# Kernel optimization log

Hardware: AMD Instinct MI355X
Metric: run time of the kernel (lower is better)

Reference implementation:

```python
import jax, jax.numpy as jnp
import numpy as np

B, S, D = 4, 1024, 768
H = 12
DK = D // H            # 64
NUM_EMB = 10
MAX_DIST = 100000.0 * 2 ** 0.5
POS_SCALE = 100000.0   # tile positions live in [0, 100000]


def setup_inputs() -> dict:
    key = jax.random.key(0)
    ks = jax.random.split(key, 12)
    query = jax.random.normal(ks[0], (B, S, D), dtype=jnp.float32)
    key_t = jax.random.normal(ks[1], (B, S, D), dtype=jnp.float32)
    value = jax.random.normal(ks[2], (B, S, D), dtype=jnp.float32)
    tile_positions = jax.random.uniform(ks[3], (B, S, 2), dtype=jnp.float32) * POS_SCALE
    # Linear weights, torch layout [out, in]; xavier_uniform init, zero bias
    lim = float(np.sqrt(6.0 / (D + D)))
    Wq = jax.random.uniform(ks[4], (D, D), minval=-lim, maxval=lim, dtype=jnp.float32)
    Wk = jax.random.uniform(ks[5], (D, D), minval=-lim, maxval=lim, dtype=jnp.float32)
    Wv = jax.random.uniform(ks[6], (D, D), minval=-lim, maxval=lim, dtype=jnp.float32)
    bq = jnp.zeros((D,), jnp.float32)
    bk = jnp.zeros((D,), jnp.float32)
    bv = jnp.zeros((D,), jnp.float32)
    emb_k = jax.random.normal(ks[7], (NUM_EMB, DK), dtype=jnp.float32)  # nn.Embedding default N(0,1)
    return {"query": query, "key": key_t, "value": value,
            "tile_positions": tile_positions,
            "Wq": Wq, "bq": bq, "Wk": Wk, "bk": bk, "Wv": Wv, "bv": bv,
            "emb_k": emb_k}


def reference(query, key, value, tile_positions, Wq, bq, Wk, bk, Wv, bv, emb_k):
    b, s, _ = query.shape
    # projections -> [B, H, S, DK]
    q = (query @ Wq.T + bq).reshape(b, s, H, DK).transpose(0, 2, 1, 3)
    k = (key   @ Wk.T + bk).reshape(b, s, H, DK).transpose(0, 2, 1, 3)
    v = (value @ Wv.T + bv).reshape(b, s, H, DK).transpose(0, 2, 1, 3)
    # pairwise distances, normalized, discretized to embedding indices
    pos = jax.lax.stop_gradient(tile_positions)
    diff = pos[:, :, None, :] - pos[:, None, :, :]          # [B,S,S,2]
    dist = jnp.sqrt(jnp.sum(diff * diff, axis=-1)) / MAX_DIST  # [B,S,S]
    idx = jnp.clip(jnp.round(dist * (NUM_EMB - 1)), 0, NUM_EMB - 1).astype(jnp.int32)
    rk = emb_k[idx]                                          # [B,S,S,DK]
    # logits: QK^T plus distance-aware key bias
    attn_logits = jnp.einsum('bhqd,bhkd->bhqk', q, k)
    attn_logits = attn_logits + jnp.einsum('bhqd,bqkd->bhqk', q, rk)
    attn_logits = attn_logits / (DK ** 0.5)
    attention = jax.nn.softmax(attn_logits, axis=-1)
    out = jnp.einsum('bhqk,bhkd->bhqd', attention, v)       # [B,H,S,DK]
    out = out.transpose(0, 2, 1, 3).reshape(b, s, -1)       # [B,S,D]
    return out
```

## Files before the change

kernel.cpp:

```cpp
#include <hip/hip_runtime.h>
#include <hip/hip_bf16.h>

#define Bsz 4
#define Ssz 1024
#define Dsz 768
#define Hn 12
#define DKsz 64
#define NUMEMB 10

#define IDX_OFF 64
#define K_OFF   4194368
#define V_OFF   10485824
#define WBF_OFF 16777280
#define XBF_OFF 20316224
#define WS_TIER_B 20316224ULL
#define WS_TIER_A 39190592ULL

#define NXz 3145728
#define NWz 589824

typedef __attribute__((ext_vector_type(8))) short short8;
typedef __attribute__((ext_vector_type(8))) float float8;
typedef __attribute__((ext_vector_type(4))) float f32x4;
typedef __attribute__((ext_vector_type(4))) unsigned int u32x4;
typedef __attribute__((ext_vector_type(4))) short s16x4;

__device__ __forceinline__ float bfbits2f(short u) {
    union { unsigned int i; float f; } v;
    v.i = ((unsigned int)(unsigned short)u) << 16;
    return v.f;
}
__device__ __forceinline__ unsigned short f2bf_bits(float f) {
    __hip_bfloat16 h = __float2bfloat16(f);
    return *reinterpret_cast<unsigned short*>(&h);
}

template<int CTRL>
__device__ __forceinline__ float dppf(float x) {
    int xi = __float_as_int(x);
    int r = __builtin_amdgcn_update_dpp(xi, xi, CTRL, 0xF, 0xF, true);
    return __int_as_float(r);
}
__device__ __forceinline__ float red_max16(float v) {
    v = fmaxf(v, dppf<0xB1>(v));
    v = fmaxf(v, dppf<0x4E>(v));
    v = fmaxf(v, dppf<0x124>(v));
    v = fmaxf(v, dppf<0x128>(v));
    return v;
}
__device__ __forceinline__ float red_sum16(float v) {
    v += dppf<0xB1>(v);
    v += dppf<0x4E>(v);
    v += dppf<0x124>(v);
    v += dppf<0x128>(v);
    return v;
}

template<bool BF16>
__device__ __forceinline__ float loadf(const void* base, size_t idx) {
    if constexpr (BF16) return __bfloat162float(((const __hip_bfloat16*)base)[idx]);
    else return ((const float*)base)[idx];
}
template<bool BF16>
__device__ __forceinline__ short8 load8bf(const void* base, size_t idx) {
    if constexpr (BF16) {
        return *(const short8*)((const short*)base + idx);
    } else {
        float8 f = *(const float8*)((const float*)base + idx);
        short8 r;
#pragma unroll
        for (int i = 0; i < 8; i++) r[i] = (short)f2bf_bits(f[i]);
        return r;
    }
}
template<bool BF16>
__device__ __forceinline__ float8 load8f(const void* base, size_t idx) {
    if constexpr (BF16) {
        short8 s = *(const short8*)((const short*)base + idx);
        float8 f;
#pragma unroll
        for (int i = 0; i < 8; i++) f[i] = bfbits2f(s[i]);
        return f;
    } else {
        return *(const float8*)((const float*)base + idx);
    }
}

__global__ __launch_bounds__(64) void detect_kernel(
    const unsigned int* __restrict__ q, const unsigned int* __restrict__ p,
    const unsigned int* __restrict__ w, const unsigned int* __restrict__ e,
    int* __restrict__ flags)
{
    const int which = blockIdx.x;
    const unsigned int* ptr = (which == 0) ? q : ((which == 1) ? p : ((which == 2) ? w : e));
    const int n = (which == 3) ? 320 : ((which == 1) ? 4096 : 1024);
    int cnt = 0;
    for (int i = threadIdx.x; i < n; i += 64) {
        const unsigned int ex = (ptr[i] >> 7) & 0xFF;
        cnt += (ex >= 110 && ex <= 145) ? 1 : 0;
    }
#pragma unroll
    for (int off = 1; off < 64; off <<= 1) cnt += __shfl_xor(cnt, off, 64);
    if (threadIdx.x == 0) flags[which] = (2 * cnt > n) ? 1 : 0;
}

__global__ __launch_bounds__(256) void conv_kernel(
    const void* __restrict__ X0, const void* __restrict__ X1, const void* __restrict__ X2,
    const void* __restrict__ W0, const void* __restrict__ W1, const void* __restrict__ W2,
    const int* __restrict__ flags, short* __restrict__ Xbf, short* __restrict__ Wbf,
    int doX)
{
    const long t = (long)blockIdx.x * 256 + threadIdx.x;
    const bool xb = flags[0] != 0, wb = flags[2] != 0;
    if (doX) {
        const long i8 = t * 8;
        if (i8 < (long)3 * NXz) {
            const int z = (int)(i8 / NXz);
            const long off = i8 - (long)z * NXz;
            const void* X = (z == 0) ? X0 : ((z == 1) ? X1 : X2);
            short8 v = xb ? load8bf<true>(X, off) : load8bf<false>(X, off);
            *(short8*)(Xbf + i8) = v;
        } else {
            const long j = i8 - (long)3 * NXz;
            const int z = (int)(j / NWz);
            const long off = j - (long)z * NWz;
            const void* W = (z == 0) ? W0 : ((z == 1) ? W1 : W2);
            short8 v = wb ? load8bf<true>(W, off) : load8bf<false>(W, off);
            *(short8*)(Wbf + j) = v;
        }
    } else {
        const long j = t * 8;
        const int z = (int)(j / NWz);
        const long off = j - (long)z * NWz;
        const void* W = (z == 0) ? W0 : ((z == 1) ? W1 : W2);
        short8 v = wb ? load8bf<true>(W, off) : load8bf<false>(W, off);
        *(short8*)(Wbf + j) = v;
    }
}

template<bool PB>
__device__ __forceinline__ void idx_body(
    const void* pos, unsigned char* __restrict__ idxb)
{
    const int kt = blockIdx.x, qt = blockIdx.y, b = blockIdx.z;
    const int t = threadIdx.x;
    const int r = t >> 2, cc = t & 3;
    const int q = qt * 64 + r;
    const float qx = loadf<PB>(pos, ((size_t)b * Ssz + q) * 2);
    const float qy = loadf<PB>(pos, ((size_t)b * Ssz + q) * 2 + 1);
    const float MAXD = 141421.35623730951f;
    const int k0 = kt * 64 + cc * 16;
    unsigned int w[4];
#pragma unroll
    for (int g = 0; g < 4; g++) {
        unsigned int acc = 0;
#pragma unroll
        for (int u = 0; u < 4; u++) {
            const int k = k0 + g * 4 + u;
            const float kx = loadf<PB>(pos, ((size_t)b * Ssz + k) * 2);
            const float ky = loadf<PB>(pos, ((size_t)b * Ssz + k) * 2 + 1);
            const float dx = __fsub_rn(qx, kx);
            const float dy = __fsub_rn(qy, ky);
            const float ss = __fadd_rn(__fmul_rn(dx, dx), __fmul_rn(dy, dy));
            const float dist = __fdiv_rn(sqrtf(ss), MAXD);
            const float d9 = __fmul_rn(dist, 9.0f);
            int idx = (int)rintf(d9);
            idx = idx < 0 ? 0 : (idx > NUMEMB - 1 ? NUMEMB - 1 : idx);
            acc |= ((unsigned int)idx) << (8 * u);
        }
        w[g] = acc;
    }
    u32x4 v; v[0] = w[0]; v[1] = w[1]; v[2] = w[2]; v[3] = w[3];
    *(u32x4*)(idxb + ((size_t)(b * Ssz + q)) * Ssz + k0) = v;
}

__global__ __launch_bounds__(256) void idx_kernel(
    const void* pos, const int* __restrict__ flags, unsigned char* __restrict__ idxb)
{
    if (flags[1] != 0) idx_body<true >(pos, idxb);
    else               idx_body<false>(pos, idxb);
}

template<bool XB, bool WB>
__device__ __forceinline__ void proj_body(
    const void* X, const void* W, const void* bias, bool biasbf, void* Y, bool ybf,
    int zmode, int bx, int by, short* As, short* Bs)
{
    const int tid  = threadIdx.x;
    const int wave = tid >> 6;
    const int lane = tid & 63;
    const int l15  = lane & 15;
    const int quad = lane >> 4;
    const int wm = wave & 1;
    const int wn = wave >> 1;
    const int m0 = bx * 64;
    const int n0 = by * 128;

    f32x4 acc[2][4];
#pragma unroll
    for (int i = 0; i < 2; i++)
#pragma unroll
        for (int j = 0; j < 4; j++) acc[i][j] = (f32x4)0.0f;

    const int r0 = tid >> 3;
    const int cc = tid & 7;

    short8 pa0 = load8bf<XB>(X, (size_t)(m0 + r0)      * Dsz + cc * 8);
    short8 pa1 = load8bf<XB>(X, (size_t)(m0 + 32 + r0) * Dsz + cc * 8);
    short8 pb0 = load8bf<WB>(W, (size_t)(n0 + r0)      * Dsz + cc * 8);
    short8 pb1 = load8bf<WB>(W, (size_t)(n0 + 32 + r0) * Dsz + cc * 8);
    short8 pb2 = load8bf<WB>(W, (size_t)(n0 + 64 + r0) * Dsz + cc * 8);
    short8 pb3 = load8bf<WB>(W, (size_t)(n0 + 96 + r0) * Dsz + cc * 8);

    for (int kk = 0; kk < Dsz; kk += 64) {
        __syncthreads();
        *(short8*)&As[(r0)      * 72 + cc * 8] = pa0;
        *(short8*)&As[(32 + r0) * 72 + cc * 8] = pa1;
        *(short8*)&Bs[(r0)      * 72 + cc * 8] = pb0;
        *(short8*)&Bs[(32 + r0) * 72 + cc * 8] = pb1;
        *(short8*)&Bs[(64 + r0) * 72 + cc * 8] = pb2;
        *(short8*)&Bs[(96 + r0) * 72 + cc * 8] = pb3;
        __syncthreads();

        if (kk + 64 < Dsz) {
            const int k2 = kk + 64 + cc * 8;
            pa0 = load8bf<XB>(X, (size_t)(m0 + r0)      * Dsz + k2);
            pa1 = load8bf<XB>(X, (size_t)(m0 + 32 + r0) * Dsz + k2);
            pb0 = load8bf<WB>(W, (size_t)(n0 + r0)      * Dsz + k2);
            pb1 = load8bf<WB>(W, (size_t)(n0 + 32 + r0) * Dsz + k2);
            pb2 = load8bf<WB>(W, (size_t)(n0 + 64 + r0) * Dsz + k2);
            pb3 = load8bf<WB>(W, (size_t)(n0 + 96 + r0) * Dsz + k2);
        }

#pragma unroll
        for (int st = 0; st < 2; st++) {
            short8 af[2], bf[4];
#pragma unroll
            for (int i = 0; i < 2; i++)
                af[i] = *(const short8*)&As[(wm * 32 + i * 16 + l15) * 72 + st * 32 + quad * 8];
#pragma unroll
            for (int j = 0; j < 4; j++)
                bf[j] = *(const short8*)&Bs[(wn * 64 + j * 16 + l15) * 72 + st * 32 + quad * 8];
#pragma unroll
            for (int i = 0; i < 2; i++)
#pragma unroll
                for (int j = 0; j < 4; j++)
                    acc[i][j] = __builtin_amdgcn_mfma_f32_16x16x32_bf16(af[i], bf[j], acc[i][j], 0, 0, 0);
        }
    }

#pragma unroll
    for (int j = 0; j < 4; j++) {
        const int n = n0 + wn * 64 + j * 16 + l15;
        const float bv_ = biasbf ? loadf<true>(bias, n) : loadf<false>(bias, n);
        const int hh = n >> 6, dk = n & 63;
#pragma unroll
        for (int i = 0; i < 2; i++) {
            const int ms = m0 + wm * 32 + i * 16 + quad * 4;
            const int bb = ms >> 10;
            const int s0 = ms & 1023;
            if (zmode == 2) {
                s16x4 pkv;
#pragma unroll
                for (int r = 0; r < 4; r++) pkv[r] = (short)f2bf_bits(acc[i][j][r] + bv_);
                *(s16x4*)((short*)Y + (((size_t)bb * Hn + hh) * DKsz + dk) * Ssz + s0) = pkv;
            } else if (zmode == 1) {
#pragma unroll
                for (int r = 0; r < 4; r++)
                    ((__hip_bfloat16*)Y)[(((size_t)bb * Hn + hh) * Ssz + (s0 + r)) * DKsz + dk] =
                        __float2bfloat16(acc[i][j][r] + bv_);
            } else {
#pragma unroll
                for (int r = 0; r < 4; r++) {
                    const float val = acc[i][j][r] + bv_;
                    const size_t oi = (size_t)(ms + r) * Dsz + n;
                    if (ybf) ((__hip_bfloat16*)Y)[oi] = __float2bfloat16(val);
                    else     ((float*)Y)[oi] = val;
                }
            }
        }
    }
}

__global__ __launch_bounds__(256) void proj_kernel(
    const void* X0, const void* X1, const void* X2,
    const void* Wq, const void* bq, const void* Wk, const void* bk,
    const void* Wv, const void* bv,
    void* Qw, void* Kw, void* Vw, const int* __restrict__ flags,
    int fx, int fw)
{
    __shared__ __align__(16) short As[64 * 72];
    __shared__ __align__(16) short Bs[128 * 72];
    const int z = blockIdx.z;
    const void* X = (z == 0) ? X0 : ((z == 1) ? X1 : X2);
    const void* W = (z == 0) ? Wq : ((z == 1) ? Wk : Wv);
    const void* B = (z == 0) ? bq : ((z == 1) ? bk : bv);
    void* Y = (z == 0) ? Qw : ((z == 1) ? Kw : Vw);
    const bool xb = fx || flags[0] != 0;
    const bool wb = fw || flags[2] != 0;
    const bool biasbf = flags[2] != 0;
    const bool ybf = (flags[0] != 0) || (z != 0);
    if (xb) { if (wb) proj_body<true , true >(X, W, B, biasbf, Y, ybf, z, blockIdx.x, blockIdx.y, As, Bs);
              else    proj_body<true , false>(X, W, B, biasbf, Y, ybf, z, blockIdx.x, blockIdx.y, As, Bs); }
    else    { if (wb) proj_body<false, true >(X, W, B, biasbf, Y, ybf, z, blockIdx.x, blockIdx.y, As, Bs);
              else    proj_body<false, false>(X, W, B, biasbf, Y, ybf, z, blockIdx.x, blockIdx.y, As, Bs); }
}

template<bool QB, bool EB>
__device__ __forceinline__ void attn_body(
    const void* Qw, const short* __restrict__ Ks, const short* __restrict__ Vs,
    const unsigned char* __restrict__ idxb, const void* __restrict__ emb, void* out,
    unsigned short* Klds, unsigned short* Vtlds, unsigned short* Plds, float* qe)
{
    const int qt = blockIdx.x, h = blockIdx.y, b = blockIdx.z;
    const int tid  = threadIdx.x;
    const int wave = tid >> 6;
    const int lane = tid & 63;
    const int l15  = lane & 15;
    const int quad = lane >> 4;

    for (int p = tid; p < 64 * NUMEMB; p += 256) {
        const int row = p / NUMEMB, e = p - row * NUMEMB;
        const size_t qoff = ((size_t)b * Ssz + qt * 64 + row) * Dsz + h * DKsz;
        float s = 0.f;
#pragma unroll
        for (int c = 0; c < 8; c++) {
            short8 qv = load8bf<QB>(Qw, qoff + c * 8);
            float8 ef = load8f<EB>(emb, (size_t)e * DKsz + c * 8);
#pragma unroll
            for (int i = 0; i < 8; i++) s += bfbits2f(qv[i]) * ef[i];
        }
        qe[p] = s;
    }

    short8 qfrag[2];
    {
        const size_t qbase = ((size_t)b * Ssz + qt * 64 + wave * 16 + l15) * Dsz + h * DKsz;
        qfrag[0] = load8bf<QB>(Qw, qbase + quad * 8);
        qfrag[1] = load8bf<QB>(Qw, qbase + 32 + quad * 8);
    }

    float m_run[4], l_run[4];
    f32x4 oacc[4];
#pragma unroll
    for (int r = 0; r < 4; r++) { m_run[r] = -1e30f; l_run[r] = 0.f; }
#pragma unroll
    for (int j = 0; j < 4; j++) oacc[j] = (f32x4)0.0f;

    const int lds_off = (tid >> 3) * 72 + (tid & 7) * 8;
    const short* kp = Ks + ((size_t)(b * Hn + h) * Ssz) * DKsz + tid * 8;
    const short* vp = Vs + ((size_t)(b * Hn + h) * DKsz + (tid >> 3)) * Ssz + (tid & 7) * 8;
    const unsigned char* ip = idxb + ((size_t)b * Ssz + l15) * Ssz
                                   + (size_t)qt * 64 + wave * 16 + quad * 4;

    short8 pk0 = *(const short8*)(kp);
    short8 pk1 = *(const short8*)(kp + 2048);
    short8 pv0 = *(const short8*)(vp);
    short8 pv1 = *(const short8*)(vp + 32 * Ssz);
    unsigned int id0 = *(const unsigned int*)(ip);
    unsigned int id1 = *(const unsigned int*)(ip + 16 * Ssz);
    unsigned int id2 = *(const unsigned int*)(ip + 32 * Ssz);
    unsigned int id3 = *(const unsigned int*)(ip + 48 * Ssz);

    *(short8*)&Klds[lds_off]           = pk0;
    *(short8*)&Klds[32 * 72 + lds_off] = pk1;
    *(short8*)&Vtlds[lds_off]           = pv0;
    *(short8*)&Vtlds[32 * 72 + lds_off] = pv1;
    __syncthreads();

    const float CSC = 0.18033688011112042f;

    for (int it = 0; it < 16; ++it) {
        const int cur = (it & 1) ? (64 * 72) : 0;
        const int nxt = (it & 1) ? 0 : (64 * 72);
        const unsigned int jd[4] = { id0, id1, id2, id3 };

        if (it + 1 < 16) {
            kp += 4096;
            vp += 64;
            ip += (size_t)64 * Ssz;
            pk0 = *(const short8*)(kp);
            pk1 = *(const short8*)(kp + 2048);
            pv0 = *(const short8*)(vp);
            pv1 = *(const short8*)(vp + 32 * Ssz);
            id0 = *(const unsigned int*)(ip);
            id1 = *(const unsigned int*)(ip + 16 * Ssz);
            id2 = *(const unsigned int*)(ip + 32 * Ssz);
            id3 = *(const unsigned int*)(ip + 48 * Ssz);
        }

        f32x4 sf[4];
#pragma unroll
        for (int j = 0; j < 4; j++) sf[j] = (f32x4)0.0f;
        __builtin_amdgcn_s_setprio(1);
#pragma unroll
        for (int st = 0; st < 2; st++) {
#pragma unroll
            for (int j = 0; j < 4; j++) {
                short8 kb2 = *(const short8*)&Klds[cur + (j * 16 + l15) * 72 + st * 32 + quad * 8];
                sf[j] = __builtin_amdgcn_mfma_f32_16x16x32_bf16(qfrag[st], kb2, sf[j], 0, 0, 0);
            }
        }
        __builtin_amdgcn_s_setprio(0);

        float sv[4][4];
#pragma unroll
        for (int j = 0; j < 4; j++) {
            const unsigned int iw = jd[j];
#pragma unroll
            for (int r = 0; r < 4; r++) {
                const int m = wave * 16 + quad * 4 + r;
                const int idx = (iw >> (8 * r)) & 0xFF;
                sv[r][j] = (sf[j][r] + qe[m * NUMEMB + idx]) * CSC;
            }
        }

        float alpha[4];
#pragma unroll
        for (int r = 0; r < 4; r++) {
            float vmax = fmaxf(fmaxf(sv[r][0], sv[r][1]), fmaxf(sv[r][2], sv[r][3]));
            vmax = red_max16(vmax);
            const float mnew = fmaxf(m_run[r], vmax);
            alpha[r] = exp2f(m_run[r] - mnew);
            m_run[r] = mnew;
            float psum = 0.f;
#pragma unroll
            for (int j = 0; j < 4; j++) {
                const float p = exp2f(sv[r][j] - mnew);
                sv[r][j] = p;
                psum += p;
            }
            psum = red_sum16(psum);
            l_run[r] = l_run[r] * alpha[r] + psum;
        }
#pragma unroll
        for (int j = 0; j < 4; j++) {
            f32x4 o = oacc[j];
#pragma unroll
            for (int r = 0; r < 4; r++) o[r] *= alpha[r];
            oacc[j] = o;
        }

#pragma unroll
        for (int r = 0; r < 4; r++) {
            const int m = wave * 16 + quad * 4 + r;
#pragma unroll
            for (int j = 0; j < 4; j++) {
                const int csw = (j * 16 + l15) ^ (quad << 4);
                Plds[m * 72 + csw] = f2bf_bits(sv[r][j]);
            }
        }

        __builtin_amdgcn_s_setprio(1);
#pragma unroll
        for (int st = 0; st < 2; st++) {
            const int prow = wave * 16 + l15;
            const int pcsw = (st * 32 + quad * 8) ^ ((l15 >> 2) << 4);
            short8 pf = *(const short8*)&Plds[prow * 72 + pcsw];
#pragma unroll
            for (int j = 0; j < 4; j++) {
                short8 vb = *(const short8*)&Vtlds[cur + (j * 16 + l15) * 72 + st * 32 + quad * 8];
                oacc[j] = __builtin_amdgcn_mfma_f32_16x16x32_bf16(pf, vb, oacc[j], 0, 0, 0);
            }
        }
        __builtin_amdgcn_s_setprio(0);

        if (it + 1 < 16) {
            *(short8*)&Klds[nxt + lds_off]           = pk0;
            *(short8*)&Klds[nxt + 32 * 72 + lds_off] = pk1;
            *(short8*)&Vtlds[nxt + lds_off]           = pv0;
            *(short8*)&Vtlds[nxt + 32 * 72 + lds_off] = pv1;
        }
        __syncthreads();
    }

#pragma unroll
    for (int r = 0; r < 4; r++) {
        const float inv = 1.0f / l_run[r];
        const int m = qt * 64 + wave * 16 + quad * 4 + r;
#pragma unroll
        for (int j = 0; j < 4; j++) {
            const int n = h * DKsz + j * 16 + l15;
            const float val = oacc[j][r] * inv;
            const size_t oidx = ((size_t)b * Ssz + m) * Dsz + n;
            if constexpr (QB) ((__hip_bfloat16*)out)[oidx] = __float2bfloat16(val);
            else              ((float*)out)[oidx] = val;
        }
    }
}

__global__ __launch_bounds__(256) void attn_kernel(
    const void* Qw, const short* __restrict__ Ks, const short* __restrict__ Vs,
    const unsigned char* __restrict__ idxb, const void* __restrict__ emb, void* out,
    const int* __restrict__ flags)
{
    __shared__ __align__(16) unsigned short Klds[2 * 64 * 72];
    __shared__ __align__(16) unsigned short Vtlds[2 * 64 * 72];
    __shared__ __align__(16) unsigned short Plds[64 * 72];
    __shared__ __align__(16) float qe[64 * NUMEMB];

    const bool qb = flags[0] != 0, eb = flags[3] != 0;
    if (qb) { if (eb) attn_body<true , true >(Qw, Ks, Vs, idxb, emb, out, Klds, Vtlds, Plds, qe);
              else    attn_body<true , false>(Qw, Ks, Vs, idxb, emb, out, Klds, Vtlds, Plds, qe); }
    else    { if (eb) attn_body<false, true >(Qw, Ks, Vs, idxb, emb, out, Klds, Vtlds, Plds, qe);
              else    attn_body<false, false>(Qw, Ks, Vs, idxb, emb, out, Klds, Vtlds, Plds, qe); }
}

extern "C" void kernel_launch(void* const* d_in, const int* in_sizes, int n_in,
                              void* d_out, int out_size, void* d_ws, size_t ws_size,
                              hipStream_t stream) {
    const void* query = d_in[0];
    const void* key   = d_in[1];
    const void* value = d_in[2];
    const void* tpos  = d_in[3];
    const void* Wq    = d_in[4];
    const void* bq    = d_in[5];
    const void* Wk    = d_in[6];
    const void* bk    = d_in[7];
    const void* Wv    = d_in[8];
    const void* bv    = d_in[9];
    const void* emb   = d_in[10];

    int*           flags = (int*)d_ws;
    unsigned char* idxb  = (unsigned char*)d_ws + IDX_OFF;
    void*          Kw    = (char*)d_ws + K_OFF;
    void*          Vw    = (char*)d_ws + V_OFF;
    short*         Wbf   = (short*)((char*)d_ws + WBF_OFF);
    short*         Xbf   = (short*)((char*)d_ws + XBF_OFF);
    void*          Qw    = d_out;

    const bool tierA = ws_size >= WS_TIER_A;
    const bool tierB = !tierA && ws_size >= WS_TIER_B;

    detect_kernel<<<4, 64, 0, stream>>>(
        (const unsigned int*)query, (const unsigned int*)tpos,
        (const unsigned int*)Wq, (const unsigned int*)emb, flags);

    if (tierA)
        conv_kernel<<<5472, 256, 0, stream>>>(query, key, value, Wq, Wk, Wv, flags, Xbf, Wbf, 1);
    else if (tierB)
        conv_kernel<<<864, 256, 0, stream>>>(query, key, value, Wq, Wk, Wv, flags, Xbf, Wbf, 0);

    idx_kernel<<<dim3(16, 16, Bsz), 256, 0, stream>>>(tpos, flags, idxb);

    if (tierA)
        proj_kernel<<<dim3(64, 6, 3), 256, 0, stream>>>(
            Xbf, Xbf + NXz, Xbf + 2 * NXz,
            Wbf, bq, Wbf + NWz, bk, Wbf + 2 * NWz, bv,
            Qw, Kw, Vw, flags, 1, 1);
    else if (tierB)
        proj_kernel<<<dim3(64, 6, 3), 256, 0, stream>>>(
            query, key, value,
            Wbf, bq, Wbf + NWz, bk, Wbf + 2 * NWz, bv,
            Qw, Kw, Vw, flags, 0, 1);
    else
        proj_kernel<<<dim3(64, 6, 3), 256, 0, stream>>>(
            query, key, value, Wq, bq, Wk, bk, Wv, bv,
            Qw, Kw, Vw, flags, 0, 0);

    attn_kernel<<<dim3(16, Hn, Bsz), 256, 0, stream>>>(
        Qw, (const short*)Kw, (const short*)Vw, idxb, emb, d_out, flags);
}
```

Baseline: 220.2 us.

## Compute transposed S=K·Q^T in registers, drop P LDS round-trip, lazy rescale

```diff
diff --git a/kernel.cpp b/kernel.cpp
--- a/kernel.cpp
+++ b/kernel.cpp
@@ -23,6 +23,7 @@
 typedef __attribute__((ext_vector_type(8))) float float8;
 typedef __attribute__((ext_vector_type(4))) float f32x4;
 typedef __attribute__((ext_vector_type(4))) unsigned int u32x4;
+typedef __attribute__((ext_vector_type(2))) unsigned int u32x2;
 typedef __attribute__((ext_vector_type(4))) short s16x4;
 
 __device__ __forceinline__ float bfbits2f(short u) {
@@ -33,27 +34,6 @@
 __device__ __forceinline__ unsigned short f2bf_bits(float f) {
     __hip_bfloat16 h = __float2bfloat16(f);
     return *reinterpret_cast<unsigned short*>(&h);
-}
-
-template<int CTRL>
-__device__ __forceinline__ float dppf(float x) {
-    int xi = __float_as_int(x);
-    int r = __builtin_amdgcn_update_dpp(xi, xi, CTRL, 0xF, 0xF, true);
-    return __int_as_float(r);
-}
-__device__ __forceinline__ float red_max16(float v) {
-    v = fmaxf(v, dppf<0xB1>(v));
-    v = fmaxf(v, dppf<0x4E>(v));
-    v = fmaxf(v, dppf<0x124>(v));
-    v = fmaxf(v, dppf<0x128>(v));
-    return v;
-}
-__device__ __forceinline__ float red_sum16(float v) {
-    v += dppf<0xB1>(v);
-    v += dppf<0x4E>(v);
-    v += dppf<0x124>(v);
-    v += dppf<0x128>(v);
-    return v;
 }
 
 template<bool BF16>
@@ -310,7 +290,7 @@
 __device__ __forceinline__ void attn_body(
     const void* Qw, const short* __restrict__ Ks, const short* __restrict__ Vs,
     const unsigned char* __restrict__ idxb, const void* __restrict__ emb, void* out,
-    unsigned short* Klds, unsigned short* Vtlds, unsigned short* Plds, float* qe)
+    unsigned short* Klds, unsigned short* Vtlds, float* qe)
 {
     const int qt = blockIdx.x, h = blockIdx.y, b = blockIdx.z;
     const int tid  = threadIdx.x;
@@ -319,6 +299,8 @@
     const int l15  = lane & 15;
     const int quad = lane >> 4;
 
+    const float CSC = 0.18033688011112042f;
+
     for (int p = tid; p < 64 * NUMEMB; p += 256) {
         const int row = p / NUMEMB, e = p - row * NUMEMB;
         const size_t qoff = ((size_t)b * Ssz + qt * 64 + row) * Dsz + h * DKsz;
@@ -330,7 +312,7 @@
 #pragma unroll
             for (int i = 0; i < 8; i++) s += bfbits2f(qv[i]) * ef[i];
         }
-        qe[p] = s;
+        qe[p] = s * CSC;
     }
 
     short8 qfrag[2];
@@ -340,148 +322,165 @@
         qfrag[1] = load8bf<QB>(Qw, qbase + 32 + quad * 8);
     }
 
-    float m_run[4], l_run[4];
+    float m_run = -1e30f, l_run = 0.f;
     f32x4 oacc[4];
 #pragma unroll
-    for (int r = 0; r < 4; r++) { m_run[r] = -1e30f; l_run[r] = 0.f; }
-#pragma unroll
     for (int j = 0; j < 4; j++) oacc[j] = (f32x4)0.0f;
 
-    const int lds_off = (tid >> 3) * 72 + (tid & 7) * 8;
+    const int r0 = tid >> 3, cc = tid & 7;
+    const int ksl = (cc + 4 * (r0 & 1) - r0) & 7;
+    const int kwoff = r0 * 72 + ksl * 8;
+    const int vwoff = r0 * 72 + cc * 8;
+
+    int koff[4][2];
+#pragma unroll
+    for (int jb = 0; jb < 4; jb++) {
+        const int krow = (jb & 2) * 16 + (l15 >> 2) * 8 + (jb & 1) * 4 + (l15 & 3);
+        const int base = quad + 4 * (l15 & 1) - (l15 & 3) + 8;
+#pragma unroll
+        for (int st = 0; st < 2; st++)
+            koff[jb][st] = krow * 72 + ((base + 4 * (st ^ (jb & 1))) & 7) * 8;
+    }
+
     const short* kp = Ks + ((size_t)(b * Hn + h) * Ssz) * DKsz + tid * 8;
-    const short* vp = Vs + ((size_t)(b * Hn + h) * DKsz + (tid >> 3)) * Ssz + (tid & 7) * 8;
-    const unsigned char* ip = idxb + ((size_t)b * Ssz + l15) * Ssz
-                                   + (size_t)qt * 64 + wave * 16 + quad * 4;
+    const short* vp = Vs + ((size_t)(b * Hn + h) * DKsz + r0) * Ssz + cc * 8;
+    const unsigned char* ip = idxb + ((size_t)b * Ssz + qt * 64 + wave * 16 + l15) * Ssz + quad * 8;
+    const int qrow10 = (wave * 16 + l15) * NUMEMB;
 
     short8 pk0 = *(const short8*)(kp);
     short8 pk1 = *(const short8*)(kp + 2048);
     short8 pv0 = *(const short8*)(vp);
     short8 pv1 = *(const short8*)(vp + 32 * Ssz);
-    unsigned int id0 = *(const unsigned int*)(ip);
-    unsigned int id1 = *(const unsigned int*)(ip + 16 * Ssz);
-    unsigned int id2 = *(const unsigned int*)(ip + 32 * Ssz);
-    unsigned int id3 = *(const unsigned int*)(ip + 48 * Ssz);
-
-    *(short8*)&Klds[lds_off]           = pk0;
-    *(short8*)&Klds[32 * 72 + lds_off] = pk1;
-    *(short8*)&Vtlds[lds_off]           = pv0;
-    *(short8*)&Vtlds[32 * 72 + lds_off] = pv1;
+    u32x2 idA = *(const u32x2*)(ip);
+    u32x2 idB = *(const u32x2*)(ip + 32);
+
+    *(short8*)&Klds[kwoff]            = pk0;
+    *(short8*)&Klds[32 * 72 + kwoff]  = pk1;
+    *(short8*)&Vtlds[vwoff]           = pv0;
+    *(short8*)&Vtlds[32 * 72 + vwoff] = pv1;
     __syncthreads();
-
-    const float CSC = 0.18033688011112042f;
 
     for (int it = 0; it < 16; ++it) {
         const int cur = (it & 1) ? (64 * 72) : 0;
         const int nxt = (it & 1) ? 0 : (64 * 72);
-        const unsigned int jd[4] = { id0, id1, id2, id3 };
+        const unsigned int jd[4] = { idA[0], idA[1], idB[0], idB[1] };
 
         if (it + 1 < 16) {
             kp += 4096;
             vp += 64;
-            ip += (size_t)64 * Ssz;
+            ip += 64;
             pk0 = *(const short8*)(kp);
             pk1 = *(const short8*)(kp + 2048);
             pv0 = *(const short8*)(vp);
             pv1 = *(const short8*)(vp + 32 * Ssz);
-            id0 = *(const unsigned int*)(ip);
-            id1 = *(const unsigned int*)(ip + 16 * Ssz);
-            id2 = *(const unsigned int*)(ip + 32 * Ssz);
-            id3 = *(const unsigned int*)(ip + 48 * Ssz);
+            idA = *(const u32x2*)(ip);
+            idB = *(const u32x2*)(ip + 32);
         }
 
         f32x4 sf[4];
 #pragma unroll
-        for (int j = 0; j < 4; j++) sf[j] = (f32x4)0.0f;
+        for (int jb = 0; jb < 4; jb++) sf[jb] = (f32x4)0.0f;
         __builtin_amdgcn_s_setprio(1);
 #pragma unroll
         for (int st = 0; st < 2; st++) {
 #pragma unroll
+            for (int jb = 0; jb < 4; jb++) {
+                short8 kf = *(const short8*)&Klds[cur + koff[jb][st]];
+                sf[jb] = __builtin_amdgcn_mfma_f32_16x16x32_bf16(kf, qfrag[st], sf[jb], 0, 0, 0);
+            }
+        }
+        __builtin_amdgcn_s_setprio(0);
+
+        float sv[4][4];
+#pragma unroll
+        for (int jb = 0; jb < 4; jb++) {
+            const unsigned int iw = jd[jb];
+#pragma unroll
+            for (int r = 0; r < 4; r++)
+                sv[jb][r] = fmaf(sf[jb][r], CSC, qe[qrow10 + ((iw >> (8 * r)) & 0xFF)]);
+        }
+
+        float t0 = fmaxf(fmaxf(sv[0][0], sv[0][1]), fmaxf(sv[0][2], sv[0][3]));
+        float t1 = fmaxf(fmaxf(sv[1][0], sv[1][1]), fmaxf(sv[1][2], sv[1][3]));
+        float t2 = fmaxf(fmaxf(sv[2][0], sv[2][1]), fmaxf(sv[2][2], sv[2][3]));
+        float t3 = fmaxf(fmaxf(sv[3][0], sv[3][1]), fmaxf(sv[3][2], sv[3][3]));
+        float vmax = fmaxf(fmaxf(t0, t1), fmaxf(t2, t3));
+        vmax = fmaxf(vmax, __shfl_xor(vmax, 16, 64));
+        vmax = fmaxf(vmax, __shfl_xor(vmax, 32, 64));
+
+        if (!__all(vmax - m_run <= 8.0f)) {
+            const float mnew = fmaxf(m_run, vmax);
+            const float alpha = exp2f(m_run - mnew);
+            m_run = mnew;
+            l_run *= alpha;
+            float aO[4];
+#pragma unroll
+            for (int r = 0; r < 4; r++)
+                aO[r] = __shfl(alpha, (lane & 48) | (quad * 4 + r), 64);
+#pragma unroll
             for (int j = 0; j < 4; j++) {
-                short8 kb2 = *(const short8*)&Klds[cur + (j * 16 + l15) * 72 + st * 32 + quad * 8];
-                sf[j] = __builtin_amdgcn_mfma_f32_16x16x32_bf16(qfrag[st], kb2, sf[j], 0, 0, 0);
+                f32x4 o = oacc[j];
+#pragma unroll
+                for (int r = 0; r < 4; r++) o[r] *= aO[r];
+                oacc[j] = o;
             }
         }
-        __builtin_amdgcn_s_setprio(0);
-
-        float sv[4][4];
-#pragma unroll
-        for (int j = 0; j < 4; j++) {
-            const unsigned int iw = jd[j];
-#pragma unroll
-            for (int r = 0; r < 4; r++) {
-                const int m = wave * 16 + quad * 4 + r;
-                const int idx = (iw >> (8 * r)) & 0xFF;
-                sv[r][j] = (sf[j][r] + qe[m * NUMEMB + idx]) * CSC;
-            }
-        }
-
-        float alpha[4];
-#pragma unroll
-        for (int r = 0; r < 4; r++) {
-            float vmax = fmaxf(fmaxf(sv[r][0], sv[r][1]), fmaxf(sv[r][2], sv[r][3]));
-            vmax = red_max16(vmax);
-            const float mnew = fmaxf(m_run[r], vmax);
-            alpha[r] = exp2f(m_run[r] - mnew);
-            m_run[r] = mnew;
-            float psum = 0.f;
-#pragma unroll
-            for (int j = 0; j < 4; j++) {
-                const float p = exp2f(sv[r][j] - mnew);
-                sv[r][j] = p;
-                psum += p;
-            }
-            psum = red_sum16(psum);
-            l_run[r] = l_run[r] * alpha[r] + psum;
-        }
-#pragma unroll
-        for (int j = 0; j < 4; j++) {
-            f32x4 o = oacc[j];
-#pragma unroll
-            for (int r = 0; r < 4; r++) o[r] *= alpha[r];
-            oacc[j] = o;
-        }
-
-#pragma unroll
-        for (int r = 0; r < 4; r++) {
-            const int m = wave * 16 + quad * 4 + r;
-#pragma unroll
-            for (int j = 0; j < 4; j++) {
-                const int csw = (j * 16 + l15) ^ (quad << 4);
-                Plds[m * 72 + csw] = f2bf_bits(sv[r][j]);
-            }
-        }
+
+#pragma unroll
+        for (int jb = 0; jb < 4; jb++)
+#pragma unroll
+            for (int r = 0; r < 4; r++)
+                sv[jb][r] = exp2f(sv[jb][r] - m_run);
+
+        float s0 = (sv[0][0] + sv[0][1]) + (sv[0][2] + sv[0][3]);
+        float s1 = (sv[1][0] + sv[1][1]) + (sv[1][2] + sv[1][3]);
+        float s2 = (sv[2][0] + sv[2][1]) + (sv[2][2] + sv[2][3]);
+        float s3 = (sv[3][0] + sv[3][1]) + (sv[3][2] + sv[3][3]);
+        float psum = (s0 + s1) + (s2 + s3);
+        psum += __shfl_xor(psum, 16, 64);
+        psum += __shfl_xor(psum, 32, 64);
+        l_run += psum;
+
+        short8 pa[2];
+#pragma unroll
+        for (int st = 0; st < 2; st++)
+#pragma unroll
+            for (int j = 0; j < 8; j++)
+                pa[st][j] = (short)f2bf_bits(sv[2 * st + (j >> 2)][j & 3]);
 
         __builtin_amdgcn_s_setprio(1);
 #pragma unroll
         for (int st = 0; st < 2; st++) {
-            const int prow = wave * 16 + l15;
-            const int pcsw = (st * 32 + quad * 8) ^ ((l15 >> 2) << 4);
-            short8 pf = *(const short8*)&Plds[prow * 72 + pcsw];
 #pragma unroll
             for (int j = 0; j < 4; j++) {
                 short8 vb = *(const short8*)&Vtlds[cur + (j * 16 + l15) * 72 + st * 32 + quad * 8];
-                oacc[j] = __builtin_amdgcn_mfma_f32_16x16x32_bf16(pf, vb, oacc[j], 0, 0, 0);
+                oacc[j] = __builtin_amdgcn_mfma_f32_16x16x32_bf16(pa[st], vb, oacc[j], 0, 0, 0);
             }
         }
         __builtin_amdgcn_s_setprio(0);
 
         if (it + 1 < 16) {
-            *(short8*)&Klds[nxt + lds_off]           = pk0;
-            *(short8*)&Klds[nxt + 32 * 72 + lds_off] = pk1;
-            *(short8*)&Vtlds[nxt + lds_off]           = pv0;
-            *(short8*)&Vtlds[nxt + 32 * 72 + lds_off] = pv1;
+            *(short8*)&Klds[nxt + kwoff]            = pk0;
+            *(short8*)&Klds[nxt + 32 * 72 + kwoff]  = pk1;
+            *(short8*)&Vtlds[nxt + vwoff]           = pv0;
+            *(short8*)&Vtlds[nxt + 32 * 72 + vwoff] = pv1;
         }
         __syncthreads();
     }
 
+    const float inv = 1.0f / l_run;
+    float invO[4];
+#pragma unroll
+    for (int r = 0; r < 4; r++)
+        invO[r] = __shfl(inv, (lane & 48) | (quad * 4 + r), 64);
+
 #pragma unroll
     for (int r = 0; r < 4; r++) {
-        const float inv = 1.0f / l_run[r];
         const int m = qt * 64 + wave * 16 + quad * 4 + r;
 #pragma unroll
         for (int j = 0; j < 4; j++) {
             const int n = h * DKsz + j * 16 + l15;
-            const float val = oacc[j][r] * inv;
+            const float val = oacc[j][r] * invO[r];
             const size_t oidx = ((size_t)b * Ssz + m) * Dsz + n;
             if constexpr (QB) ((__hip_bfloat16*)out)[oidx] = __float2bfloat16(val);
             else              ((float*)out)[oidx] = val;
@@ -496,14 +495,13 @@
 {
     __shared__ __align__(16) unsigned short Klds[2 * 64 * 72];
     __shared__ __align__(16) unsigned short Vtlds[2 * 64 * 72];
-    __shared__ __align__(16) unsigned short Plds[64 * 72];
     __shared__ __align__(16) float qe[64 * NUMEMB];
 
     const bool qb = flags[0] != 0, eb = flags[3] != 0;
-    if (qb) { if (eb) attn_body<true , true >(Qw, Ks, Vs, idxb, emb, out, Klds, Vtlds, Plds, qe);
-              else    attn_body<true , false>(Qw, Ks, Vs, idxb, emb, out, Klds, Vtlds, Plds, qe); }
-    else    { if (eb) attn_body<false, true >(Qw, Ks, Vs, idxb, emb, out, Klds, Vtlds, Plds, qe);
-              else    attn_body<false, false>(Qw, Ks, Vs, idxb, emb, out, Klds, Vtlds, Plds, qe); }
+    if (qb) { if (eb) attn_body<true , true >(Qw, Ks, Vs, idxb, emb, out, Klds, Vtlds, qe);
+              else    attn_body<true , false>(Qw, Ks, Vs, idxb, emb, out, Klds, Vtlds, qe); }
+    else    { if (eb) attn_body<false, true >(Qw, Ks, Vs, idxb, emb, out, Klds, Vtlds, qe);
+              else    attn_body<false, false>(Qw, Ks, Vs, idxb, emb, out, Klds, Vtlds, qe); }
 }
 
 extern "C" void kernel_launch(void* const* d_in, const int* in_sizes, int n_in,
```

After: 207.5 us. -5.8%, faster.
